# Kernel tuning notes

Hardware: AMD Instinct MI355X
Metric: run time of the kernel (lower is better)

Reference implementation:

```python
import jax, jax.numpy as jnp
import numpy as np

B, S, D, H = 4, 2048, 512, 8
HD = D // H  # head_dim = 64


def setup_inputs() -> dict:
    key = jax.random.key(0)
    ks = jax.random.split(key, 16)
    sd = 1.0 / np.sqrt(D)
    def lin(ka, kb):
        W = jax.random.uniform(ka, (D, D), jnp.float32, -sd, sd)
        b = jax.random.uniform(kb, (D,), jnp.float32, -sd, sd)
        return W, b
    Wq, bq = lin(ks[0], ks[1])
    Wk, bk = lin(ks[2], ks[3])
    Wv, bv = lin(ks[4], ks[5])
    Wo, bo = lin(ks[6], ks[7])
    Ws, bs = lin(ks[8], ks[9])
    Wsh, bsh = lin(ks[10], ks[11])
    mod1_feat = jax.random.normal(ks[12], (B, S, D), jnp.float32)
    mod2_feat = jax.random.normal(ks[13], (B, S, D), jnp.float32)
    return {"mod1_feat": mod1_feat, "mod2_feat": mod2_feat,
            "Wq": Wq, "bq": bq, "Wk": Wk, "bk": bk, "Wv": Wv, "bv": bv,
            "Wo": Wo, "bo": bo, "Ws": Ws, "bs": bs, "Wsh": Wsh, "bsh": bsh}


def _heads(x):
    # [B, S, D] -> [B, H, S, HD]
    b, s, _ = x.shape
    return x.reshape(b, s, H, HD).transpose(0, 2, 1, 3)


def reference(mod1_feat, mod2_feat, Wq, bq, Wk, bk, Wv, bv, Wo, bo, Ws, bs, Wsh, bsh):
    Q = _heads(mod1_feat @ Wq + bq)
    K = _heads(mod2_feat @ Wk + bk)
    V = _heads(mod2_feat @ Wv + bv)
    scale = _heads(mod2_feat @ Ws + bs)
    shift = _heads(mod2_feat @ Wsh + bsh)
    K = K * scale + shift
    V = V * scale + shift
    scores = jnp.einsum('bhqd,bhkd->bhqk', Q, K) / jnp.sqrt(jnp.float32(HD))
    attn = jax.nn.softmax(scores, axis=-1)
    out = jnp.einsum('bhqk,bhkd->bhqd', attn, V)  # [B, H, S, HD]
    out = out.transpose(0, 2, 1, 3).reshape(mod1_feat.shape[0], -1, H * HD)
    return out @ Wo + bo
```

## Files before the change

### kernel.cpp

```cpp
#include <hip/hip_runtime.h>
#include <hip/hip_bf16.h>
#include <cstdint>
#include <cstddef>

typedef __bf16 bf16_t;
typedef __bf16 bf16x8 __attribute__((ext_vector_type(8)));
typedef __bf16 bf16x4 __attribute__((ext_vector_type(4)));
typedef float f32x4 __attribute__((ext_vector_type(4)));

#define DEVINL static __device__ __forceinline__

constexpr int B_ = 4, S_ = 2048, D_ = 512, H_ = 8, HD_ = 64;
constexpr int M_ = B_ * S_;
constexpr int NIN = 14;

DEVINL bf16x8 load8g(const bf16_t* p) { return *reinterpret_cast<const bf16x8*>(p); }

DEVINL int swcol(int col, int row) {
  return (col & ~63) | ((((col >> 3) ^ row) & 7) << 3) | (col & 7);
}

DEVINL int pK(int row) { return (row & 3) | (((row >> 3) & 1) << 2); }
DEVINL int swcolK(int col, int row) {
  return (col & ~63) | ((((col >> 3) ^ pK(row)) & 7) << 3) | (col & 7);
}

DEVINL void gl2lds(const bf16_t* g, bf16_t* l) {
  __builtin_amdgcn_global_load_lds(
      (const __attribute__((address_space(1))) void*)g,
      (__attribute__((address_space(3))) void*)l, 16, 0, 0);
}

DEVINL void stage16(bf16_t* dst, const void* src, size_t off, bool f32) {
  if (f32) {
    const float* p = (const float*)src + off;
    bf16x8 v0, v1;
#pragma unroll
    for (int j = 0; j < 8; ++j) { v0[j] = (bf16_t)p[j]; v1[j] = (bf16_t)p[8 + j]; }
    *reinterpret_cast<bf16x8*>(dst)     = v0;
    *reinterpret_cast<bf16x8*>(dst + 8) = v1;
  } else {
    const bf16_t* p = (const bf16_t*)src + off;
    *reinterpret_cast<bf16x8*>(dst)     = load8g(p);
    *reinterpret_cast<bf16x8*>(dst + 8) = load8g(p + 8);
  }
}

DEVINL float readf(const void* p, size_t i, bool f32) {
  return f32 ? ((const float*)p)[i] : (float)((const bf16_t*)p)[i];
}

struct DetectArgs { const uint16_t* p[NIN]; int n[NIN]; int* flags; };

__global__ __launch_bounds__(64) void detect_kernel(DetectArgs a) {
  const int z = blockIdx.x;
  const uint16_t* p = a.p[z];
  const int n = a.n[z];
  const int t = threadIdx.x;
  int cnt = 0;
  for (int i = t; i < n; i += 64) {
    const int e = (p[i] >> 7) & 0xFF;
    cnt += (e >= 200);
  }
#pragma unroll
  for (int off = 32; off > 0; off >>= 1) cnt += __shfl_down(cnt, off, 64);
  if (t == 0) a.flags[z] = (cnt > 16) ? 1 : 0;
}

struct PrepArgs {
  const void* csrc[2]; bf16_t* cdst[2]; int cidx[2];
  const void* wsrc[6]; int wIdx[6]; bf16_t* wdst[6];
  const int* flags;
};

__global__ __launch_bounds__(256) void prep_kernel(PrepArgs a) {
  __shared__ bf16_t tile[64][80];
  const int bid = blockIdx.x;
  if (bid < 4096) {
    const int z = bid >> 11;
    const int bx = bid & 2047;
    const bool f32 = a.flags[a.cidx[z]] != 0;
    const size_t i = ((size_t)bx * 256 + threadIdx.x) * 8;
    const int row = (int)(i >> 9);
    const int col = (int)(i & 511);
    bf16_t* dst = a.cdst[z] + (size_t)row * 512 + swcol(col, row);
    if (f32) {
      const float* p = (const float*)a.csrc[z] + i;
      bf16x8 v;
#pragma unroll
      for (int j = 0; j < 8; ++j) v[j] = (bf16_t)p[j];
      *reinterpret_cast<bf16x8*>(dst) = v;
    } else {
      *reinterpret_cast<bf16x8*>(dst) = load8g((const bf16_t*)a.csrc[z] + i);
    }
  } else {
    const int rem = bid - 4096;
    const int w = rem >> 6;
    const int r6 = rem & 63;
    const int k0 = (r6 & 7) * 64, n0 = (r6 >> 3) * 64;
    const void* src = a.wsrc[w];
    const bool f32 = a.flags[a.wIdx[w]] != 0;
    bf16_t* dst = a.wdst[w];
    const int t = threadIdx.x;
    const int r = t >> 2, c0 = (t & 3) * 16;
    stage16(&tile[r][c0], src, (size_t)(k0 + r) * 512 + n0 + c0, f32);
    __syncthreads();
    const int orow = n0 + r;
    bf16_t* o = dst + (size_t)orow * 512;
#pragma unroll
    for (int half = 0; half < 2; ++half) {
      bf16x8 ov;
#pragma unroll
      for (int j = 0; j < 8; ++j) ov[j] = tile[c0 + half * 8 + j][r];
      *reinterpret_cast<bf16x8*>(o + swcol(k0 + c0 + half * 8, orow)) = ov;
    }
  }
}

struct GemmBatch {
  const bf16_t* A[3];
  const bf16_t* Bt[3];
  const void* bias[3]; int bIdx[3];
  void* C[3];          int cIdx[3];
  const int* flags;
};

__global__ __launch_bounds__(512) void gemm_bt_kernel(GemmBatch args) {
  constexpr int K = 512, N = 512;
  __shared__ bf16_t As[3][128][64];
  __shared__ bf16_t Bs[3][64][64];
  const int z = blockIdx.z;
  const bf16_t* Ag  = args.A[z];
  const bf16_t* Btg = args.Bt[z];
  const int m0 = blockIdx.x * 128, n0 = blockIdx.y * 64;
  const int t = threadIdx.x, lane = t & 63, wave = t >> 6;
  const int l16 = lane & 15, quad = lane >> 4;
  const int wm = wave * 16;
  const int lr = lane >> 3, lc = (lane & 7) * 8;

  auto stage = [&](int slot, int k0) {
#pragma unroll
    for (int s = 0; s < 2; ++s) {
      const int r = wm + s * 8;
      gl2lds(Ag + (size_t)(m0 + r + lr) * K + k0 + lc, &As[slot][r][0]);
    }
    gl2lds(Btg + (size_t)(n0 + wave * 8 + lr) * K + k0 + lc, &Bs[slot][wave * 8][0]);
  };

  f32x4 acc[4] = {};

  stage(0, 0);
  stage(1, 64);

  constexpr int NT = K / 64;
  int cur = 0;
  for (int kt = 0; kt < NT - 1; ++kt) {
    asm volatile("s_waitcnt vmcnt(3)\n\ts_barrier" ::: "memory");
    __builtin_amdgcn_sched_barrier(0);
    if (kt + 2 < NT) {
      const int slot2 = cur == 0 ? 2 : cur - 1;
      stage(slot2, (kt + 2) * 64);
    }
#pragma unroll
    for (int ks = 0; ks < 2; ++ks) {
      const int sw = swcol(ks * 32 + quad * 8, l16);
      bf16x8 af = *reinterpret_cast<const bf16x8*>(&As[cur][wm + l16][sw]);
      bf16x8 bfr[4];
#pragma unroll
      for (int j = 0; j < 4; ++j)
        bfr[j] = *reinterpret_cast<const bf16x8*>(&Bs[cur][j * 16 + l16][sw]);
#pragma unroll
      for (int j = 0; j < 4; ++j)
        acc[j] = __builtin_amdgcn_mfma_f32_16x16x32_bf16(af, bfr[j], acc[j], 0, 0, 0);
    }
    cur = (cur == 2) ? 0 : cur + 1;
  }
  asm volatile("s_waitcnt vmcnt(0)\n\ts_barrier" ::: "memory");
  __builtin_amdgcn_sched_barrier(0);
#pragma unroll
  for (int ks = 0; ks < 2; ++ks) {
    const int sw = swcol(ks * 32 + quad * 8, l16);
    bf16x8 af = *reinterpret_cast<const bf16x8*>(&As[cur][wm + l16][sw]);
    bf16x8 bfr[4];
#pragma unroll
    for (int j = 0; j < 4; ++j)
      bfr[j] = *reinterpret_cast<const bf16x8*>(&Bs[cur][j * 16 + l16][sw]);
#pragma unroll
    for (int j = 0; j < 4; ++j)
      acc[j] = __builtin_amdgcn_mfma_f32_16x16x32_bf16(af, bfr[j], acc[j], 0, 0, 0);
  }

  const void* biag = args.bias[z];
  void* Cg         = args.C[z];
  const bool bf32 = args.bIdx[z] >= 0 && args.flags[args.bIdx[z]];
  const bool cf32 = args.cIdx[z] >= 0 && args.flags[args.cIdx[z]];
#pragma unroll
  for (int j = 0; j < 4; ++j) {
    const int col = n0 + j * 16 + l16;
    const float bv = readf(biag, col, bf32);
    const int rowb = m0 + wm + quad * 4;
#pragma unroll
    for (int r = 0; r < 4; ++r) {
      const size_t idx = (size_t)(rowb + r) * N + col;
      const float v = acc[j][r] + bv;
      if (cf32) ((float*)Cg)[idx] = v;
      else      ((bf16_t*)Cg)[idx] = (bf16_t)v;
    }
  }
}

struct KsvArgs {
  const bf16_t* A;
  const bf16_t* Bt[4];
  const void* bias[4]; int bIdx[4];
  bf16_t* Kmod;
  bf16_t* VtT;
  const int* flags;
};

__global__ __launch_bounds__(1024) void ksv_kernel(KsvArgs args) {
  constexpr int K = 512;
  __shared__ bf16_t As[3][128][64];
  __shared__ bf16_t Bs[3][4][64][64];
  const int m0 = blockIdx.x * 128, n0 = blockIdx.y * 64;
  const int t = threadIdx.x, lane = t & 63, wave = t >> 6;
  const int l16 = lane & 15, quad = lane >> 4;
  const int wm = (wave >> 2) * 32;
  const int wn = (wave & 3) * 16;
  const int lr = lane >> 3, lc = (lane & 7) * 8;

  auto stage = [&](int slot, int k0) {
    gl2lds(args.A + (size_t)(m0 + wave * 8 + lr) * K + k0 + lc, &As[slot][wave * 8][0]);
    const int mat = wave >> 2;
    const int rb = (wave & 3) * 16;
#pragma unroll
    for (int s = 0; s < 2; ++s) {
      const int r = rb + s * 8;
      gl2lds(args.Bt[mat] + (size_t)(n0 + r + lr) * K + k0 + lc, &Bs[slot][mat][r][0]);
    }
  };

  f32x4 acc[4][2] = {};

  stage(0, 0);
  stage(1, 64);

  constexpr int NT = K / 64;
  int cur = 0;
  for (int kt = 0; kt < NT - 1; ++kt) {
    asm volatile("s_waitcnt vmcnt(3)\n\ts_barrier" ::: "memory");
    __builtin_amdgcn_sched_barrier(0);
    if (kt + 2 < NT) {
      const int slot2 = cur == 0 ? 2 : cur - 1;
      stage(slot2, (kt + 2) * 64);
    }
#pragma unroll
    for (int ks = 0; ks < 2; ++ks) {
      const int sw = swcol(ks * 32 + quad * 8, l16);
      bf16x8 af[2], bfr[4];
#pragma unroll
      for (int mi = 0; mi < 2; ++mi)
        af[mi] = *reinterpret_cast<const bf16x8*>(&As[cur][wm + mi * 16 + l16][sw]);
#pragma unroll
      for (int mat = 0; mat < 4; ++mat)
        bfr[mat] = *reinterpret_cast<const bf16x8*>(&Bs[cur][mat][wn + l16][sw]);
#pragma unroll
      for (int mat = 0; mat < 4; ++mat)
#pragma unroll
        for (int mi = 0; mi < 2; ++mi)
          acc[mat][mi] = __builtin_amdgcn_mfma_f32_16x16x32_bf16(af[mi], bfr[mat], acc[mat][mi], 0, 0, 0);
    }
    cur = (cur == 2) ? 0 : cur + 1;
  }
  asm volatile("s_waitcnt vmcnt(0)\n\ts_barrier" ::: "memory");
  __builtin_amdgcn_sched_barrier(0);
#pragma unroll
  for (int ks = 0; ks < 2; ++ks) {
    const int sw = swcol(ks * 32 + quad * 8, l16);
    bf16x8 af[2], bfr[4];
#pragma unroll
    for (int mi = 0; mi < 2; ++mi)
      af[mi] = *reinterpret_cast<const bf16x8*>(&As[cur][wm + mi * 16 + l16][sw]);
#pragma unroll
    for (int mat = 0; mat < 4; ++mat)
      bfr[mat] = *reinterpret_cast<const bf16x8*>(&Bs[cur][mat][wn + l16][sw]);
#pragma unroll
    for (int mat = 0; mat < 4; ++mat)
#pragma unroll
      for (int mi = 0; mi < 2; ++mi)
        acc[mat][mi] = __builtin_amdgcn_mfma_f32_16x16x32_bf16(af[mi], bfr[mat], acc[mat][mi], 0, 0, 0);
  }

  const int col = n0 + wn + l16;
  const float bk  = readf(args.bias[0], col, args.bIdx[0] >= 0 && args.flags[args.bIdx[0]]);
  const float bv  = readf(args.bias[1], col, args.bIdx[1] >= 0 && args.flags[args.bIdx[1]]);
  const float bs  = readf(args.bias[2], col, args.bIdx[2] >= 0 && args.flags[args.bIdx[2]]);
  const float bsh = readf(args.bias[3], col, args.bIdx[3] >= 0 && args.flags[args.bIdx[3]]);
  const int hh = col >> 6, dd = col & 63;
#pragma unroll
  for (int mi = 0; mi < 2; ++mi) {
    const int rowb = m0 + wm + mi * 16 + quad * 4;
    bf16x4 vpack;
#pragma unroll
    for (int r = 0; r < 4; ++r) {
      const int row = rowb + r;
      const float s  = acc[2][mi][r] + bs;
      const float sh = acc[3][mi][r] + bsh;
      const float kk = fmaf(acc[0][mi][r] + bk, s, sh);
      const float vv = fmaf(acc[1][mi][r] + bv, s, sh);
      args.Kmod[(size_t)row * 512 + swcolK(col, row)] = (bf16_t)kk;
      vpack[r] = (bf16_t)vv;
    }
    const int bb = rowb >> 11;
    const int ss = rowb & 2047;
    *reinterpret_cast<bf16x4*>(
        args.VtT + (((size_t)(bb * H_ + hh)) * HD_ + dd) * S_ + swcol(ss, dd)) = vpack;
  }
}

__global__ __launch_bounds__(512) void attn_kernel(const bf16_t* M1, const bf16_t* Wq,
                                                   const void* bq, const int* flags,
                                                   const bf16_t* Kb, const bf16_t* Vt,
                                                   bf16_t* O) {
  __shared__ bf16_t Ks[3][64][64];
  __shared__ bf16_t Vs[3][64][64];
  __shared__ bf16_t Xs[3][64][64];
  const int i = blockIdx.x;
  const int xcd = i & 7, g = i >> 3;
  const int slice = xcd * 4 + (g & 3);
  const int qt = g >> 2;
  const int b = slice >> 3, h = slice & 7;
  const int t = threadIdx.x, wave = t >> 6, lane = t & 63;
  const int l16 = lane & 15, quad = lane >> 4;
  const int q0 = qt * 128 + wave * 16;
  const int lr = lane >> 3, lc = (lane & 7) * 8;

  const size_t q0g = (size_t)b * S_ + qt * 128;

  auto qstage = [&](int set, int k0) {
#pragma unroll
    for (int s = 0; s < 2; ++s) {
      const int r = wave * 16 + s * 8;
      bf16_t* dst = (wave < 4) ? &Ks[set][r][0] : &Vs[set][r - 64][0];
      gl2lds(M1 + (q0g + r + lr) * D_ + k0 + lc, dst);
    }
    gl2lds(Wq + (size_t)(h * HD_ + wave * 8 + lr) * D_ + k0 + lc, &Xs[set][wave * 8][0]);
  };

  f32x4 qacc[4] = {};
  const bf16_t* brow = (wave < 4) ? &Ks[0][wave * 16][0] : &Vs[0][wave * 16 - 64][0];
  const int setstride = 64 * 64;

  auto qcompute = [&](int set) {
    const bf16_t* bbase = brow + set * setstride;
#pragma unroll
    for (int ks = 0; ks < 2; ++ks) {
      const int sw = swcol(ks * 32 + quad * 8, l16);
      bf16x8 bf = *reinterpret_cast<const bf16x8*>(bbase + l16 * 64 + sw);
      bf16x8 af[4];
#pragma unroll
      for (int j = 0; j < 4; ++j)
        af[j] = *reinterpret_cast<const bf16x8*>(&Xs[set][j * 16 + l16][sw]);
#pragma unroll
      for (int j = 0; j < 4; ++j)
        qacc[j] = __builtin_amdgcn_mfma_f32_16x16x32_bf16(af[j], bf, qacc[j], 0, 0, 0);
    }
  };

  qstage(0, 0);
  qstage(1, 64);
  {
    constexpr int QNT = D_ / 64;
    int cur = 0;
    for (int kt = 0; kt < QNT - 1; ++kt) {
      asm volatile("s_waitcnt vmcnt(3)\n\ts_barrier" ::: "memory");
      __builtin_amdgcn_sched_barrier(0);
      if (kt + 2 < QNT) {
        const int slot2 = cur == 0 ? 2 : cur - 1;
        qstage(slot2, (kt + 2) * 64);
      }
      qcompute(cur);
      cur = (cur == 2) ? 0 : cur + 1;
    }
    asm volatile("s_waitcnt vmcnt(0)\n\ts_barrier" ::: "memory");
    __builtin_amdgcn_sched_barrier(0);
    qcompute(cur);
  }
  const bool qbf32 = flags[3] != 0;
  __syncthreads();
  bf16_t* qls = &Xs[0][0][0];
#pragma unroll
  for (int j = 0; j < 4; ++j) {
    bf16x4 pk;
#pragma unroll
    for (int r = 0; r < 4; ++r) {
      const int d = j * 16 + quad * 4 + r;
      pk[r] = (bf16_t)(qacc[j][r] + readf(bq, h * HD_ + d, qbf32));
    }
    *reinterpret_cast<bf16x4*>(&qls[wave * 1024 + l16 * 64 + swcol(j * 16 + quad * 4, l16)]) = pk;
  }
  __syncthreads();
  bf16x8 qf[2];
#pragma unroll
  for (int dc = 0; dc < 2; ++dc)
    qf[dc] = *reinterpret_cast<const bf16x8*>(&qls[wave * 1024 + l16 * 64 + swcol(dc * 32 + quad * 8, l16)]);

  bf16x8 ones;
#pragma unroll
  for (int j = 0; j < 8; ++j) ones[j] = (bf16_t)1.0f;

  f32x4 oacc[4] = {};
  f32x4 lacc = {};

  const size_t kbase = (size_t)b * S_ * D_ + h * HD_;
  const size_t vbase = ((size_t)(b * H_ + h)) * HD_ * S_;

  const int rbase = ((l16 >> 2) << 3) | (l16 & 3);
  int koff[2][4];
#pragma unroll
  for (int j = 0; j < 4; ++j) {
    const int rho = rbase + (j >> 1) * 32 + (j & 1) * 4;
#pragma unroll
    for (int dc = 0; dc < 2; ++dc)
      koff[dc][j] = rho * 64 + swcolK(dc * 32 + quad * 8, rho);
  }
  const int voff[2] = { swcol(quad * 8, l16), swcol(32 + quad * 8, l16) };

  auto stage = [&](int slot, int k0) {
    const int r = wave * 8;
    gl2lds(Kb + kbase + (size_t)(k0 + r + lr) * D_ + lc, &Ks[slot][r][0]);
    gl2lds(Vt + vbase + (size_t)(r + lr) * S_ + k0 + lc, &Vs[slot][r][0]);
  };

  constexpr float CE = 0.18033688011112042f;

  auto compute = [&](int cur) {
    f32x4 sacc[4] = {};
    const bf16_t* ksbase = &Ks[cur][0][0];
#pragma unroll
    for (int dc = 0; dc < 2; ++dc) {
      bf16x8 kf[4];
#pragma unroll
      for (int j = 0; j < 4; ++j)
        kf[j] = *reinterpret_cast<const bf16x8*>(ksbase + koff[dc][j]);
#pragma unroll
      for (int j = 0; j < 4; ++j)
        sacc[j] = __builtin_amdgcn_mfma_f32_16x16x32_bf16(kf[j], qf[dc], sacc[j], 0, 0, 0);
    }
#pragma unroll
    for (int kc = 0; kc < 2; ++kc) {
      bf16x8 vf[4];
#pragma unroll
      for (int dj = 0; dj < 4; ++dj)
        vf[dj] = *reinterpret_cast<const bf16x8*>(&Vs[cur][dj * 16 + l16][voff[kc]]);
      bf16x8 bp;
#pragma unroll
      for (int r = 0; r < 4; ++r) {
        bp[r]     = (bf16_t)__builtin_amdgcn_exp2f(fminf(sacc[kc * 2][r]     * CE, 57.5f));
        bp[4 + r] = (bf16_t)__builtin_amdgcn_exp2f(fminf(sacc[kc * 2 + 1][r] * CE, 57.5f));
      }
#pragma unroll
      for (int dj = 0; dj < 4; ++dj)
        oacc[dj] = __builtin_amdgcn_mfma_f32_16x16x32_bf16(vf[dj], bp, oacc[dj], 0, 0, 0);
      lacc = __builtin_amdgcn_mfma_f32_16x16x32_bf16(ones, bp, lacc, 0, 0, 0);
    }
  };

  asm volatile("s_waitcnt vmcnt(0)" ::: "memory");
  stage(0, 0);
  stage(1, 64);

  constexpr int NT = S_ / 64;
  int cur = 0;
  for (int kt = 0; kt < NT - 1; ++kt) {
    asm volatile("s_waitcnt vmcnt(2)\n\ts_barrier" ::: "memory");
    __builtin_amdgcn_sched_barrier(0);
    if (kt + 2 < NT) {
      const int slot2 = cur == 0 ? 2 : cur - 1;
      stage(slot2, (kt + 2) * 64);
    }
    compute(cur);
    cur = (cur == 2) ? 0 : cur + 1;
  }
  asm volatile("s_waitcnt vmcnt(0)\n\ts_barrier" ::: "memory");
  __builtin_amdgcn_sched_barrier(0);
  compute(cur);

  {
    const float linv = 1.0f / fmaxf(lacc[0], 1e-30f);
    const int q = q0 + l16;
    const size_t orow = ((size_t)b * S_ + q) * D_ + h * HD_;
#pragma unroll
    for (int dj = 0; dj < 4; ++dj) {
      bf16x4 pack;
#pragma unroll
      for (int r = 0; r < 4; ++r) pack[r] = (bf16_t)(oacc[dj][r] * linv);
      *reinterpret_cast<bf16x4*>(&O[orow + swcol(dj * 16 + quad * 4, q)]) = pack;
    }
  }
}

extern "C" void kernel_launch(void* const* d_in, const int* in_sizes, int n_in,
                              void* d_out, int out_size, void* d_ws, size_t ws_size,
                              hipStream_t stream) {
  (void)n_in; (void)out_size; (void)ws_size;

  char* ws = (char*)d_ws;
  auto alloc = [&](size_t bytes) -> char* {
    char* p = ws; ws += (bytes + 255) & ~(size_t)255; return p;
  };
  int* flags = (int*)alloc(64 * sizeof(int));
  const size_t wbytes = (size_t)512 * 512 * sizeof(bf16_t);
  const size_t fbytes = (size_t)M_ * D_ * sizeof(bf16_t);
  bf16_t* wt    = (bf16_t*)alloc(6 * wbytes);
  bf16_t* m1b   = (bf16_t*)alloc(fbytes);
  bf16_t* m2b   = (bf16_t*)alloc(fbytes);
  bf16_t* vtb   = (bf16_t*)alloc(fbytes);
  bf16_t* atmp  = (bf16_t*)alloc(fbytes);
  bf16_t* kmod  = (bf16_t*)alloc(fbytes);
  bf16_t* attn_b = atmp;

  bf16_t* wtq  = wt + 0 * 512 * 512;
  bf16_t* wtk  = wt + 1 * 512 * 512;
  bf16_t* wtv  = wt + 2 * 512 * 512;
  bf16_t* wts  = wt + 3 * 512 * 512;
  bf16_t* wtsh = wt + 4 * 512 * 512;
  bf16_t* wto  = wt + 5 * 512 * 512;

  DetectArgs da;
  for (int i = 0; i < NIN; ++i) {
    da.p[i] = (const uint16_t*)d_in[i];
    da.n[i] = in_sizes[i] < 2048 ? in_sizes[i] : 2048;
  }
  da.flags = flags;
  hipLaunchKernelGGL(detect_kernel, dim3(NIN), dim3(64), 0, stream, da);

  PrepArgs pa;
  pa.csrc[0] = d_in[0]; pa.cdst[0] = m1b; pa.cidx[0] = 0;
  pa.csrc[1] = d_in[1]; pa.cdst[1] = m2b; pa.cidx[1] = 1;
  const int widx[6] = {2, 4, 6, 10, 12, 8};
  bf16_t* wdst[6] = {wtq, wtk, wtv, wts, wtsh, wto};
  for (int i = 0; i < 6; ++i) { pa.wsrc[i] = d_in[widx[i]]; pa.wIdx[i] = widx[i]; pa.wdst[i] = wdst[i]; }
  pa.flags = flags;
  hipLaunchKernelGGL(prep_kernel, dim3(4096 + 384), dim3(256), 0, stream, pa);

  KsvArgs kv;
  kv.A = m2b;
  kv.Bt[0] = wtk; kv.Bt[1] = wtv; kv.Bt[2] = wts; kv.Bt[3] = wtsh;
  kv.bias[0] = d_in[5];  kv.bIdx[0] = 5;
  kv.bias[1] = d_in[7];  kv.bIdx[1] = 7;
  kv.bias[2] = d_in[11]; kv.bIdx[2] = 11;
  kv.bias[3] = d_in[13]; kv.bIdx[3] = 13;
  kv.Kmod = kmod; kv.VtT = vtb;
  kv.flags = flags;
  hipLaunchKernelGGL(ksv_kernel, dim3(M_ / 128, 8), dim3(1024), 0, stream, kv);

  hipLaunchKernelGGL(attn_kernel, dim3(512), dim3(512), 0, stream,
                     m1b, wtq, d_in[3], flags, kmod, vtb, attn_b);

  GemmBatch g2;
  for (int i = 0; i < 3; ++i) {
    g2.A[i] = attn_b;
    g2.Bt[i] = wto;
    g2.bias[i] = d_in[9]; g2.bIdx[i] = 9;
    g2.C[i] = d_out; g2.cIdx[i] = 0;
  }
  g2.flags = flags;
  hipLaunchKernelGGL(gemm_bt_kernel, dim3(M_ / 128, 8, 1), dim3(512), 0, stream, g2);
}
```

Before: 194.9 us.

## Fuse dtype detection into prep kernel and fold softmax scale into Q

Removes the separate detect kernel launch: each prep block now runs its own dtype detection with a block reduction, and the flags needed later are written by extra blocks appended to the prep grid. The feature-conversion blocks now handle 16 elements per thread with vectorized f32x4 loads, which halves the block count. The softmax exponent scale is multiplied into Q once at bf16 packing instead of per score in the inner loop, which saves a multiply per exp but rounds the scaled Q to bf16. The cost is redundant detection reads in every prep block.

```diff
diff --git a/kernel.cpp b/kernel.cpp
--- a/kernel.cpp
+++ b/kernel.cpp
@@ -50,58 +50,64 @@
   return f32 ? ((const float*)p)[i] : (float)((const bf16_t*)p)[i];
 }
 
-struct DetectArgs { const uint16_t* p[NIN]; int n[NIN]; int* flags; };
-
-__global__ __launch_bounds__(64) void detect_kernel(DetectArgs a) {
-  const int z = blockIdx.x;
-  const uint16_t* p = a.p[z];
-  const int n = a.n[z];
+DEVINL bool block_detect(const uint16_t* p, int n, int* dsum) {
   const int t = threadIdx.x;
   int cnt = 0;
-  for (int i = t; i < n; i += 64) {
-    const int e = (p[i] >> 7) & 0xFF;
-    cnt += (e >= 200);
-  }
+  for (int i = t; i < n; i += 256) cnt += (((p[i] >> 7) & 0xFF) >= 200);
 #pragma unroll
   for (int off = 32; off > 0; off >>= 1) cnt += __shfl_down(cnt, off, 64);
-  if (t == 0) a.flags[z] = (cnt > 16) ? 1 : 0;
+  if ((t & 63) == 0) dsum[t >> 6] = cnt;
+  __syncthreads();
+  const int tot = dsum[0] + dsum[1] + dsum[2] + dsum[3];
+  __syncthreads();
+  return tot > 16;
 }
 
 struct PrepArgs {
-  const void* csrc[2]; bf16_t* cdst[2]; int cidx[2];
-  const void* wsrc[6]; int wIdx[6]; bf16_t* wdst[6];
-  const int* flags;
+  const void* csrc[2]; bf16_t* cdst[2];
+  const void* wsrc[6]; bf16_t* wdst[6];
+  const uint16_t* dp[NIN]; int dn[NIN];
+  int* flags;
 };
 
 __global__ __launch_bounds__(256) void prep_kernel(PrepArgs a) {
   __shared__ bf16_t tile[64][80];
+  __shared__ int dsum[4];
   const int bid = blockIdx.x;
-  if (bid < 4096) {
-    const int z = bid >> 11;
-    const int bx = bid & 2047;
-    const bool f32 = a.flags[a.cidx[z]] != 0;
-    const size_t i = ((size_t)bx * 256 + threadIdx.x) * 8;
+  const int t = threadIdx.x;
+  if (bid < 2048) {
+    const int z = bid >> 10;
+    const bool f32 = block_detect((const uint16_t*)a.csrc[z], 2048, dsum);
+    const size_t i = ((size_t)(bid & 1023) * 256 + t) * 16;
     const int row = (int)(i >> 9);
     const int col = (int)(i & 511);
-    bf16_t* dst = a.cdst[z] + (size_t)row * 512 + swcol(col, row);
+    bf16_t* dst = a.cdst[z] + (size_t)row * 512;
+    bf16x8 v0, v1;
     if (f32) {
       const float* p = (const float*)a.csrc[z] + i;
-      bf16x8 v;
-#pragma unroll
-      for (int j = 0; j < 8; ++j) v[j] = (bf16_t)p[j];
-      *reinterpret_cast<bf16x8*>(dst) = v;
+      const f32x4 f0 = *reinterpret_cast<const f32x4*>(p);
+      const f32x4 f1 = *reinterpret_cast<const f32x4*>(p + 4);
+      const f32x4 f2 = *reinterpret_cast<const f32x4*>(p + 8);
+      const f32x4 f3 = *reinterpret_cast<const f32x4*>(p + 12);
+#pragma unroll
+      for (int j = 0; j < 4; ++j) {
+        v0[j] = (bf16_t)f0[j]; v0[4 + j] = (bf16_t)f1[j];
+        v1[j] = (bf16_t)f2[j]; v1[4 + j] = (bf16_t)f3[j];
+      }
     } else {
-      *reinterpret_cast<bf16x8*>(dst) = load8g((const bf16_t*)a.csrc[z] + i);
-    }
-  } else {
-    const int rem = bid - 4096;
+      const bf16_t* p = (const bf16_t*)a.csrc[z] + i;
+      v0 = load8g(p); v1 = load8g(p + 8);
+    }
+    *reinterpret_cast<bf16x8*>(dst + swcol(col, row))     = v0;
+    *reinterpret_cast<bf16x8*>(dst + swcol(col + 8, row)) = v1;
+  } else if (bid < 2432) {
+    const int rem = bid - 2048;
     const int w = rem >> 6;
     const int r6 = rem & 63;
     const int k0 = (r6 & 7) * 64, n0 = (r6 >> 3) * 64;
     const void* src = a.wsrc[w];
-    const bool f32 = a.flags[a.wIdx[w]] != 0;
+    const bool f32 = block_detect((const uint16_t*)src, 2048, dsum);
     bf16_t* dst = a.wdst[w];
-    const int t = threadIdx.x;
     const int r = t >> 2, c0 = (t & 3) * 16;
     stage16(&tile[r][c0], src, (size_t)(k0 + r) * 512 + n0 + c0, f32);
     __syncthreads();
@@ -114,6 +120,10 @@
       for (int j = 0; j < 8; ++j) ov[j] = tile[c0 + half * 8 + j][r];
       *reinterpret_cast<bf16x8*>(o + swcol(k0 + c0 + half * 8, orow)) = ov;
     }
+  } else {
+    const int z = bid - 2432;
+    const bool f32 = block_detect(a.dp[z], a.dn[z], dsum);
+    if (t == 0) a.flags[z] = f32 ? 1 : 0;
   }
 }
 
@@ -335,6 +345,8 @@
   const int q0 = qt * 128 + wave * 16;
   const int lr = lane >> 3, lc = (lane & 7) * 8;
 
+  constexpr float CE = 0.18033688011112042f;
+
   const size_t q0g = (size_t)b * S_ + qt * 128;
 
   auto qstage = [&](int set, int k0) {
@@ -395,7 +407,7 @@
 #pragma unroll
     for (int r = 0; r < 4; ++r) {
       const int d = j * 16 + quad * 4 + r;
-      pk[r] = (bf16_t)(qacc[j][r] + readf(bq, h * HD_ + d, qbf32));
+      pk[r] = (bf16_t)((qacc[j][r] + readf(bq, h * HD_ + d, qbf32)) * CE);
     }
     *reinterpret_cast<bf16x4*>(&qls[wave * 1024 + l16 * 64 + swcol(j * 16 + quad * 4, l16)]) = pk;
   }
@@ -432,8 +444,6 @@
     gl2lds(Vt + vbase + (size_t)(r + lr) * S_ + k0 + lc, &Vs[slot][r][0]);
   };
 
-  constexpr float CE = 0.18033688011112042f;
-
   auto compute = [&](int cur) {
     f32x4 sacc[4] = {};
     const bf16_t* ksbase = &Ks[cur][0][0];
@@ -456,8 +466,8 @@
       bf16x8 bp;
 #pragma unroll
       for (int r = 0; r < 4; ++r) {
-        bp[r]     = (bf16_t)__builtin_amdgcn_exp2f(fminf(sacc[kc * 2][r]     * CE, 57.5f));
-        bp[4 + r] = (bf16_t)__builtin_amdgcn_exp2f(fminf(sacc[kc * 2 + 1][r] * CE, 57.5f));
+        bp[r]     = (bf16_t)__builtin_amdgcn_exp2f(fminf(sacc[kc * 2][r],     57.5f));
+        bp[4 + r] = (bf16_t)__builtin_amdgcn_exp2f(fminf(sacc[kc * 2 + 1][r], 57.5f));
       }
 #pragma unroll
       for (int dj = 0; dj < 4; ++dj)
@@ -527,22 +537,18 @@
   bf16_t* wtsh = wt + 4 * 512 * 512;
   bf16_t* wto  = wt + 5 * 512 * 512;
 
-  DetectArgs da;
-  for (int i = 0; i < NIN; ++i) {
-    da.p[i] = (const uint16_t*)d_in[i];
-    da.n[i] = in_sizes[i] < 2048 ? in_sizes[i] : 2048;
-  }
-  da.flags = flags;
-  hipLaunchKernelGGL(detect_kernel, dim3(NIN), dim3(64), 0, stream, da);
-
   PrepArgs pa;
-  pa.csrc[0] = d_in[0]; pa.cdst[0] = m1b; pa.cidx[0] = 0;
-  pa.csrc[1] = d_in[1]; pa.cdst[1] = m2b; pa.cidx[1] = 1;
+  pa.csrc[0] = d_in[0]; pa.cdst[0] = m1b;
+  pa.csrc[1] = d_in[1]; pa.cdst[1] = m2b;
   const int widx[6] = {2, 4, 6, 10, 12, 8};
   bf16_t* wdst[6] = {wtq, wtk, wtv, wts, wtsh, wto};
-  for (int i = 0; i < 6; ++i) { pa.wsrc[i] = d_in[widx[i]]; pa.wIdx[i] = widx[i]; pa.wdst[i] = wdst[i]; }
+  for (int i = 0; i < 6; ++i) { pa.wsrc[i] = d_in[widx[i]]; pa.wdst[i] = wdst[i]; }
+  for (int i = 0; i < NIN; ++i) {
+    pa.dp[i] = (const uint16_t*)d_in[i];
+    pa.dn[i] = in_sizes[i] < 2048 ? in_sizes[i] : 2048;
+  }
   pa.flags = flags;
-  hipLaunchKernelGGL(prep_kernel, dim3(4096 + 384), dim3(256), 0, stream, pa);
+  hipLaunchKernelGGL(prep_kernel, dim3(2048 + 384 + 14), dim3(256), 0, stream, pa);
 
   KsvArgs kv;
   kv.A = m2b;
```

After: 191.6 us (median of 2 runs). About the same (-1.7%).
